# Kernel tuning notes

Hardware: AMD Instinct MI355X
Metric: run time of the kernel (lower is better)

Reference implementation:

```python
import jax, jax.numpy as jnp
import numpy as np

MARGIN = 1.0
N, D = 8192, 128
NUM_CLASSES = 1024


def setup_inputs() -> dict:
    key = jax.random.key(0)
    k1, k2, k3 = jax.random.split(key, 3)
    a = jax.random.normal(k1, (N, D), dtype=jnp.float32)
    b = jax.random.normal(k2, (N, D), dtype=jnp.float32)
    # L2-normalize embeddings (standard for metric learning; keeps exp() stable)
    a = a / jnp.linalg.norm(a, axis=1, keepdims=True)
    b = b / jnp.linalg.norm(b, axis=1, keepdims=True)
    labels = jax.random.randint(k3, (N,), 0, NUM_CLASSES, dtype=jnp.int64 if jax.config.jax_enable_x64 else jnp.int32)
    return {"a": a, "b": b, "labels": labels}


def reference(a, b, labels):
    # S[i, j] = a_i . b_j  -- full pairwise similarity, one GEMM
    S = a @ b.T  # [N, N]
    same = labels[:, None] == labels[None, :]  # [N, N]
    eye = jnp.eye(labels.shape[0], dtype=bool)
    pos_mask = same & ~eye          # ordered positive pairs (i != j, same label)
    neg_mask = ~same                # ordered negative pairs (labels differ)
    # V[i] = sum_k in neg(i) exp(margin + S[i, k])
    V = jnp.sum(jnp.where(neg_mask, jnp.exp(MARGIN + S), 0.0), axis=1)  # [N]
    # per positive pair (i, j): max(log(V_i + V_j) - S_ij, 0)^2
    hinge = jnp.maximum(jnp.log(V[:, None] + V[None, :]) - S, 0.0)
    comp = jnp.where(pos_mask, hinge * hinge, 0.0)
    num_pos = jnp.sum(pos_mask)
    loss = jnp.sum(comp) / (2.0 * num_pos.astype(S.dtype))
    return loss
```

## Files before the change

### kernel.cpp

```cpp
#include <hip/hip_runtime.h>

#define NN 8192
#define DD 128
#define MARGINF 1.0f
#define MAXCLS 64
#define NCHUNK 8
#define LOG2E 1.4426950408889634f
#define E1    2.718281828459045f

typedef __attribute__((ext_vector_type(8))) short bf16x8;
typedef __attribute__((ext_vector_type(4))) float f32x4;

__device__ __forceinline__ void load16_lds(const unsigned short* g, unsigned short* l) {
    __builtin_amdgcn_global_load_lds(
        (const __attribute__((address_space(1))) unsigned int*)g,
        (__attribute__((address_space(3))) unsigned int*)l,
        16, 0, 0);
}

__device__ __forceinline__ unsigned short f2bf(float x) {
    unsigned u = __float_as_uint(x);
    u = (u + 0x7FFFu + ((u >> 16) & 1u)) >> 16;
    return (unsigned short)u;
}

__global__ __launch_bounds__(256) void ml_convert_kernel(
    const float* __restrict__ a, const float* __restrict__ b,
    const int* __restrict__ labels,
    unsigned short* __restrict__ abf, unsigned short* __restrict__ bbf,
    int* __restrict__ cnt, int* __restrict__ list)
{
    int t = blockIdx.x * 256 + threadIdx.x;
    const float* src = a;
    unsigned short* dst = abf;
    int idx = t;
    float scale = LOG2E;
    if (t >= 262144) { src = b; dst = bbf; idx = t - 262144; scale = 1.0f; }
    float4 v = ((const float4*)src)[idx];
    ushort4 o;
    o.x = f2bf(v.x * scale); o.y = f2bf(v.y * scale);
    o.z = f2bf(v.z * scale); o.w = f2bf(v.w * scale);
    ((ushort4*)dst)[idx] = o;

    if (t < NN) {
        int c = labels[t];
        int p = atomicAdd(&cnt[c], 1);
        if (p < MAXCLS) list[c * MAXCLS + p] = t;
    }
}

__global__ __launch_bounds__(256, 2) void ml_vsum_gemm_kernel(
    const unsigned short* __restrict__ abf, const unsigned short* __restrict__ bbf,
    float* __restrict__ Vp)
{
    __shared__ unsigned short As[128 * DD];
    __shared__ unsigned short Bs[128 * DD];
    __shared__ float red[2][64];

    const int tid  = threadIdx.x;
    const int lane = tid & 63;
    const int wv   = tid >> 6;
    const int row0 = blockIdx.y * 128;
    const int chunk = blockIdx.x;

    const int lr = lane >> 4;
    const int p  = lane & 15;
    const int m  = lane & 15;
    const int q  = lane >> 4;
    const int xr = m & 7;

#pragma unroll
    for (int i = 0; i < 8; i++) {
        int rb = wv * 32 + i * 4;
        int r  = rb + lr;
        int c  = p ^ (r & 7);
        load16_lds(&abf[(size_t)(row0 + r) * DD + c * 8], &As[rb * DD]);
    }
    {
        int j0 = chunk * 1024;
#pragma unroll
        for (int i = 0; i < 8; i++) {
            int rb = wv * 32 + i * 4;
            int r  = rb + lr;
            int c  = p ^ (r & 7);
            load16_lds(&bbf[(size_t)(j0 + r) * DD + c * 8], &Bs[rb * DD]);
        }
    }
    __syncthreads();

    const int wi = (wv >> 1) * 64;
    const int wj = (wv & 1) * 64;

    bf16x8 afr[4][4];
#pragma unroll
    for (int ti = 0; ti < 4; ti++)
#pragma unroll
        for (int ks = 0; ks < 4; ks++) {
            int r   = wi + ti * 16 + m;
            int pos = (ks * 4 + q) ^ xr;
            afr[ti][ks] = *(const bf16x8*)(&As[r * DD + pos * 8]);
        }

    float rs[4][4];
#pragma unroll
    for (int ti = 0; ti < 4; ti++)
#pragma unroll
        for (int rg = 0; rg < 4; rg++) rs[ti][rg] = 0.f;

    const f32x4 zero = {0.f, 0.f, 0.f, 0.f};

#pragma unroll 1
    for (int jt = 0; jt < 8; jt++) {
        f32x4 acc[4][4];
#pragma unroll
        for (int ti = 0; ti < 4; ti++)
#pragma unroll
            for (int tj = 0; tj < 4; tj++) acc[ti][tj] = zero;

#pragma unroll
        for (int ks = 0; ks < 4; ks++) {
            bf16x8 bfr[4];
#pragma unroll
            for (int tj = 0; tj < 4; tj++) {
                int r   = wj + tj * 16 + m;
                int pos = (ks * 4 + q) ^ xr;
                bfr[tj] = *(const bf16x8*)(&Bs[r * DD + pos * 8]);
            }
#pragma unroll
            for (int ti = 0; ti < 4; ti++)
#pragma unroll
                for (int tj = 0; tj < 4; tj++)
                    acc[ti][tj] = __builtin_amdgcn_mfma_f32_16x16x32_bf16(afr[ti][ks], bfr[tj], acc[ti][tj], 0, 0, 0);
        }

#pragma unroll
        for (int ti = 0; ti < 4; ti++)
#pragma unroll
            for (int tj = 0; tj < 4; tj++) {
                f32x4 c = acc[ti][tj];
                rs[ti][0] += exp2f(c[0]);
                rs[ti][1] += exp2f(c[1]);
                rs[ti][2] += exp2f(c[2]);
                rs[ti][3] += exp2f(c[3]);
            }

        __syncthreads();
        if (jt < 7) {
            int j0 = chunk * 1024 + (jt + 1) * 128;
#pragma unroll
            for (int i = 0; i < 8; i++) {
                int rb = wv * 32 + i * 4;
                int r  = rb + lr;
                int c  = p ^ (r & 7);
                load16_lds(&bbf[(size_t)(j0 + r) * DD + c * 8], &Bs[rb * DD]);
            }
        }
        __syncthreads();
    }

#pragma unroll
    for (int ti = 0; ti < 4; ti++)
#pragma unroll
        for (int rg = 0; rg < 4; rg++) {
            float v = rs[ti][rg];
            v += __shfl_xor(v, 1);
            v += __shfl_xor(v, 2);
            v += __shfl_xor(v, 4);
            v += __shfl_xor(v, 8);
            rs[ti][rg] = v;
        }

    if ((wv & 1) == 1 && m == 0) {
#pragma unroll
        for (int ti = 0; ti < 4; ti++)
#pragma unroll
            for (int rg = 0; rg < 4; rg++)
                red[wv >> 1][ti * 16 + q * 4 + rg] = rs[ti][rg];
    }
    __syncthreads();
    if ((wv & 1) == 0 && m == 0) {
#pragma unroll
        for (int ti = 0; ti < 4; ti++)
#pragma unroll
            for (int rg = 0; rg < 4; rg++) {
                int rloc = ti * 16 + q * 4 + rg;
                Vp[(size_t)chunk * NN + row0 + wi + rloc] = rs[ti][rg] + red[wv >> 1][rloc];
            }
    }
}

__global__ __launch_bounds__(256) void ml_pairs_kernel(
    const float* __restrict__ a, const float* __restrict__ b,
    const int* __restrict__ cnt, const int* __restrict__ list,
    const float* __restrict__ Vp,
    float* __restrict__ classLoss, int* __restrict__ classCnt,
    unsigned int* __restrict__ done, float* __restrict__ out)
{
    __shared__ int   mem[MAXCLS];
    __shared__ float sumExp[MAXCLS];
    __shared__ float Vadj[MAXCLS];
    __shared__ float Sc[MAXCLS * MAXCLS];
    __shared__ float ps[4];
    __shared__ int   cs[4];
    __shared__ double dred[4];
    __shared__ long long cred[4];

    const int c   = blockIdx.x;
    const int tid = threadIdx.x;
    int mc = cnt[c];
    if (mc > MAXCLS) mc = MAXCLS;

    float vsum = 0.f;
    if (tid < mc) {
        int r = list[c * MAXCLS + tid];
        mem[tid] = r;
#pragma unroll
        for (int jc = 0; jc < NCHUNK; jc++) vsum += Vp[(size_t)jc * NN + r];
    }
    if (tid < MAXCLS) sumExp[tid] = 0.f;
    __syncthreads();

    const int g = tid >> 4;
    const int l = tid & 15;
    const int tot1 = mc * mc;
    for (int pp = g; pp < tot1; pp += 16) {
        int i = pp / mc;
        int j = pp - i * mc;
        int ri = mem[i], rj = mem[j];
        const float4* ar = (const float4*)(a + (size_t)ri * DD) + l * 2;
        const float4* br = (const float4*)(b + (size_t)rj * DD) + l * 2;
        float4 a0 = ar[0], a1 = ar[1];
        float4 b0 = br[0], b1 = br[1];
        float s = 0.f;
        s = fmaf(a0.x, b0.x, s); s = fmaf(a0.y, b0.y, s);
        s = fmaf(a0.z, b0.z, s); s = fmaf(a0.w, b0.w, s);
        s = fmaf(a1.x, b1.x, s); s = fmaf(a1.y, b1.y, s);
        s = fmaf(a1.z, b1.z, s); s = fmaf(a1.w, b1.w, s);
        s += __shfl_xor(s, 1);
        s += __shfl_xor(s, 2);
        s += __shfl_xor(s, 4);
        s += __shfl_xor(s, 8);
        if (l == 0) {
            Sc[i * MAXCLS + j] = s;
            atomicAdd(&sumExp[i], __expf(s));
        }
    }
    __syncthreads();

    if (tid < mc) Vadj[tid] = E1 * (vsum - sumExp[tid]);
    __syncthreads();

    float partial = 0.f;
    int   count   = 0;
    for (int pp = tid; pp < tot1; pp += 256) {
        int i = pp / mc;
        int j = pp - i * mc;
        if (i != j) {
            float h = fmaxf(logf(Vadj[i] + Vadj[j]) - Sc[i * MAXCLS + j], 0.f);
            partial += h * h;
            count++;
        }
    }
    for (int off = 32; off > 0; off >>= 1) {
        partial += __shfl_down(partial, off);
        count   += __shfl_down(count, off);
    }
    const int lane = tid & 63, wv = tid >> 6;
    if (lane == 0) { ps[wv] = partial; cs[wv] = count; }
    __syncthreads();

    if (tid == 0) {
        float tot = ps[0] + ps[1] + ps[2] + ps[3];
        int   ct  = cs[0] + cs[1] + cs[2] + cs[3];
        atomicExch(&classLoss[c], tot);
        atomicExch(&classCnt[c], ct);
    }
    __syncthreads();

    if (tid == 0) ps[0] = (float)atomicAdd(done, 1u);
    __syncthreads();
    if ((unsigned)ps[0] == 1023u) {
        double dls = 0.0;
        long long dct = 0;
        for (int k = tid; k < 1024; k += 256) {
            dls += (double)atomicAdd(&classLoss[k], 0.0f);
            dct += (long long)atomicAdd(&classCnt[k], 0);
        }
        for (int off = 32; off > 0; off >>= 1) {
            dls += __shfl_down(dls, off);
            dct += __shfl_down(dct, off);
        }
        if (lane == 0) { dred[wv] = dls; cred[wv] = dct; }
        __syncthreads();
        if (tid == 0) {
            double ls = dred[0] + dred[1] + dred[2] + dred[3];
            long long np = cred[0] + cred[1] + cred[2] + cred[3];
            out[0] = (float)(ls / (2.0 * (double)np));
        }
    }
}

extern "C" void kernel_launch(void* const* d_in, const int* in_sizes, int n_in,
                              void* d_out, int out_size, void* d_ws, size_t ws_size,
                              hipStream_t stream)
{
    const float* a      = (const float*)d_in[0];
    const float* b      = (const float*)d_in[1];
    const int*   labels = (const int*)d_in[2];
    float* out = (float*)d_out;

    char* ws = (char*)d_ws;
    unsigned short* abf = (unsigned short*)ws;
    unsigned short* bbf = (unsigned short*)(ws + 2097152);
    char*     base2     = ws + 4194304;
    int*      cnt       = (int*)(base2);
    unsigned* done      = (unsigned*)(base2 + 4096);
    float*    classLoss = (float*)(base2 + 8192);
    int*      classCnt  = (int*)(base2 + 12288);
    int*      list      = (int*)(base2 + 16384);
    float*    Vp        = (float*)(base2 + 278528);

    hipMemsetAsync(base2, 0, 4100, stream);

    ml_convert_kernel<<<2048, 256, 0, stream>>>(a, b, labels, abf, bbf, cnt, list);

    dim3 g(NCHUNK, NN / 128);
    ml_vsum_gemm_kernel<<<g, 256, 0, stream>>>(abf, bbf, Vp);

    ml_pairs_kernel<<<1024, 256, 0, stream>>>(a, b, cnt, list, Vp, classLoss, classCnt, done, out);
}
```

Baseline: 122.2 us.

## Double-buffer B tiles in the V-sum GEMM and use raw exp2 intrinsic

The B tile in the V-sum GEMM kernel is split into two 64-row LDS buffers. Each iteration computes on one buffer while the async global-to-LDS load for the tile two steps ahead goes into the buffer just consumed, which drops one of the two barriers per iteration. This hides the B load latency behind the MFMA and exp work. The per-wave tile shrinks from 4x4 to 4x2 MFMA blocks and the loop now runs 16 iterations, so there are more loop and sync steps, each with less compute. exp2f is replaced by the hardware exp2 builtin, which skips the library's range and denormal handling.

```diff
diff --git a/kernel.cpp b/kernel.cpp
--- a/kernel.cpp
+++ b/kernel.cpp
@@ -10,6 +10,12 @@
 
 typedef __attribute__((ext_vector_type(8))) short bf16x8;
 typedef __attribute__((ext_vector_type(4))) float f32x4;
+
+#if __has_builtin(__builtin_amdgcn_exp2f)
+#define EXP2F(x) __builtin_amdgcn_exp2f(x)
+#else
+#define EXP2F(x) exp2f(x)
+#endif
 
 __device__ __forceinline__ void load16_lds(const unsigned short* g, unsigned short* l) {
     __builtin_amdgcn_global_load_lds(
@@ -54,14 +60,14 @@
     float* __restrict__ Vp)
 {
     __shared__ unsigned short As[128 * DD];
-    __shared__ unsigned short Bs[128 * DD];
+    __shared__ unsigned short Bs[2][64 * DD];
     __shared__ float red[2][64];
 
     const int tid  = threadIdx.x;
     const int lane = tid & 63;
     const int wv   = tid >> 6;
     const int row0 = blockIdx.y * 128;
-    const int chunk = blockIdx.x;
+    const int j0   = blockIdx.x * 1024;
 
     const int lr = lane >> 4;
     const int p  = lane & 15;
@@ -73,23 +79,27 @@
     for (int i = 0; i < 8; i++) {
         int rb = wv * 32 + i * 4;
         int r  = rb + lr;
-        int c  = p ^ (r & 7);
-        load16_lds(&abf[(size_t)(row0 + r) * DD + c * 8], &As[rb * DD]);
-    }
-    {
-        int j0 = chunk * 1024;
-#pragma unroll
-        for (int i = 0; i < 8; i++) {
-            int rb = wv * 32 + i * 4;
-            int r  = rb + lr;
-            int c  = p ^ (r & 7);
-            load16_lds(&bbf[(size_t)(j0 + r) * DD + c * 8], &Bs[rb * DD]);
-        }
+        int cc = p ^ (r & 7);
+        load16_lds(&abf[(size_t)(row0 + r) * DD + cc * 8], &As[rb * DD]);
+    }
+#pragma unroll
+    for (int i = 0; i < 4; i++) {
+        int rb = wv * 16 + i * 4;
+        int r  = rb + lr;
+        int cc = p ^ (r & 7);
+        load16_lds(&bbf[(size_t)(j0 + r) * DD + cc * 8], &Bs[0][rb * DD]);
+    }
+#pragma unroll
+    for (int i = 0; i < 4; i++) {
+        int rb = wv * 16 + i * 4;
+        int r  = rb + lr;
+        int cc = p ^ (r & 7);
+        load16_lds(&bbf[(size_t)(j0 + 64 + r) * DD + cc * 8], &Bs[1][rb * DD]);
     }
     __syncthreads();
 
     const int wi = (wv >> 1) * 64;
-    const int wj = (wv & 1) * 64;
+    const int wj = (wv & 1) * 32;
 
     bf16x8 afr[4][4];
 #pragma unroll
@@ -109,53 +119,53 @@
 
     const f32x4 zero = {0.f, 0.f, 0.f, 0.f};
 
-#pragma unroll 1
-    for (int jt = 0; jt < 8; jt++) {
-        f32x4 acc[4][4];
+#pragma unroll 2
+    for (int jt = 0; jt < 16; jt++) {
+        const int pb = jt & 1;
+        f32x4 acc[4][2];
 #pragma unroll
         for (int ti = 0; ti < 4; ti++)
 #pragma unroll
-            for (int tj = 0; tj < 4; tj++) acc[ti][tj] = zero;
+            for (int tj = 0; tj < 2; tj++) acc[ti][tj] = zero;
 
 #pragma unroll
         for (int ks = 0; ks < 4; ks++) {
-            bf16x8 bfr[4];
-#pragma unroll
-            for (int tj = 0; tj < 4; tj++) {
+            bf16x8 bfr[2];
+#pragma unroll
+            for (int tj = 0; tj < 2; tj++) {
                 int r   = wj + tj * 16 + m;
                 int pos = (ks * 4 + q) ^ xr;
-                bfr[tj] = *(const bf16x8*)(&Bs[r * DD + pos * 8]);
+                bfr[tj] = *(const bf16x8*)(&Bs[pb][r * DD + pos * 8]);
             }
 #pragma unroll
             for (int ti = 0; ti < 4; ti++)
 #pragma unroll
-                for (int tj = 0; tj < 4; tj++)
+                for (int tj = 0; tj < 2; tj++)
                     acc[ti][tj] = __builtin_amdgcn_mfma_f32_16x16x32_bf16(afr[ti][ks], bfr[tj], acc[ti][tj], 0, 0, 0);
         }
 
 #pragma unroll
         for (int ti = 0; ti < 4; ti++)
 #pragma unroll
-            for (int tj = 0; tj < 4; tj++) {
+            for (int tj = 0; tj < 2; tj++) {
                 f32x4 c = acc[ti][tj];
-                rs[ti][0] += exp2f(c[0]);
-                rs[ti][1] += exp2f(c[1]);
-                rs[ti][2] += exp2f(c[2]);
-                rs[ti][3] += exp2f(c[3]);
+                rs[ti][0] += EXP2F(c[0]);
+                rs[ti][1] += EXP2F(c[1]);
+                rs[ti][2] += EXP2F(c[2]);
+                rs[ti][3] += EXP2F(c[3]);
             }
 
         __syncthreads();
-        if (jt < 7) {
-            int j0 = chunk * 1024 + (jt + 1) * 128;
-#pragma unroll
-            for (int i = 0; i < 8; i++) {
-                int rb = wv * 32 + i * 4;
+        if (jt < 14) {
+            int jb = j0 + (jt + 2) * 64;
+#pragma unroll
+            for (int i = 0; i < 4; i++) {
+                int rb = wv * 16 + i * 4;
                 int r  = rb + lr;
-                int c  = p ^ (r & 7);
-                load16_lds(&bbf[(size_t)(j0 + r) * DD + c * 8], &Bs[rb * DD]);
+                int cc = p ^ (r & 7);
+                load16_lds(&bbf[(size_t)(jb + r) * DD + cc * 8], &Bs[pb][rb * DD]);
             }
         }
-        __syncthreads();
     }
 
 #pragma unroll
@@ -184,7 +194,7 @@
 #pragma unroll
             for (int rg = 0; rg < 4; rg++) {
                 int rloc = ti * 16 + q * 4 + rg;
-                Vp[(size_t)chunk * NN + row0 + wi + rloc] = rs[ti][rg] + red[wv >> 1][rloc];
+                Vp[(size_t)blockIdx.x * NN + row0 + wi + rloc] = rs[ti][rg] + red[wv >> 1][rloc];
             }
     }
 }
```

New measurement: 113.6 us. 1.08x faster.
